# Kernel optimization log

Hardware: AMD Instinct MI355X
Metric: run time of the kernel (lower is better)

The kernel has to match this reference:

```python
import jax, jax.numpy as jnp
import numpy as np

B, S, K, N = 2, 4096, 4096, 4096
BLOCKSIZE = 128  # GPTQ group size


def _unpack_rows(q):
    # int32 [K//8, N] -> int32 [K, N], 8 nibbles packed along dim 0 (little-endian)
    shifts = (jnp.arange(8, dtype=jnp.int32) * 4)
    nib = (q[:, None, :] >> shifts[None, :, None]) & 0xF  # [K//8, 8, N]
    return nib.reshape(q.shape[0] * 8, q.shape[1])


def _unpack_cols(q):
    # int32 [G, N//8] -> int32 [G, N], 8 nibbles packed along dim 1
    shifts = (jnp.arange(8, dtype=jnp.int32) * 4)
    nib = (q[:, :, None] >> shifts[None, None, :]) & 0xF  # [G, N//8, 8]
    return nib.reshape(q.shape[0], q.shape[1] * 8)


def _dequant(qweight, scales, qzeros, blocksize):
    # GPTQ int4 dequant: w[k, n] = (q[k, n] - z[g, n]) * s[g, n], g = k // blocksize
    w_int = _unpack_rows(qweight).astype(jnp.float32)          # [K, N]
    zeros = _unpack_cols(qzeros).astype(jnp.float32)           # [G, N]
    z = jnp.repeat(zeros, blocksize, axis=0)                   # [K, N]
    s = jnp.repeat(scales, blocksize, axis=0)                  # [K, N]
    return (w_int - z) * s


def setup_inputs() -> dict:
    key = jax.random.key(0)
    ks = jax.random.split(key, 6)
    inp = jax.random.normal(ks[0], (B, S, K), dtype=jnp.float32)
    residual = jax.random.normal(ks[1], (B, S, N), dtype=jnp.float32)
    qweight = jax.random.randint(ks[2], (K // 8, N), 0, 2147483647, dtype=jnp.int32)
    qzeros = jax.random.randint(ks[3], (K // BLOCKSIZE, N // 8), 0, 2147483647, dtype=jnp.int32)
    scales = jax.random.uniform(ks[4], (K // BLOCKSIZE, N), dtype=jnp.float32, minval=1e-3, maxval=1e-2)
    bias = jax.random.normal(ks[5], (N,), dtype=jnp.float32)
    return {"input": inp, "residual": residual, "qweight": qweight,
            "scales": scales, "qzeros": qzeros, "bias": bias}


def reference(input, residual, qweight, scales, qzeros, bias):
    # Fused: dequant(int4 GPTQ) -> GEMM -> +bias -> +residual (mm_bias_add_int4)
    w = _dequant(qweight, scales, qzeros, BLOCKSIZE)           # [K, N]
    out = jnp.einsum('bsk,kn->bsn', input, w) + bias + residual
    return out
```

## Files before the change

### kernel.cpp

```cpp
#include <hip/hip_runtime.h>
#include <hip/hip_bf16.h>
#include <stdint.h>

using bf16 = __hip_bfloat16;
typedef __attribute__((ext_vector_type(8))) short short8;
typedef __attribute__((ext_vector_type(4))) float floatx4;

#define DEVINL __device__ __forceinline__

constexpr int K_DIM = 4096;
constexpr int N_DIM = 4096;
constexpr int M_DIM = 8192;

constexpr int BM = 128, BN = 128, BK = 64;
constexpr int NBLK_N = N_DIM / BN;
constexpr int NBLK_M = M_DIM / BM;

DEVINL void gload_lds16(const void* g, void* l) {
  __builtin_amdgcn_global_load_lds((const __attribute__((address_space(1))) void*)g,
                                   (__attribute__((address_space(3))) void*)l,
                                   16, 0, 0);
}

__global__ __launch_bounds__(256) void k_a_convert(const float* __restrict__ a,
                                                   bf16* __restrict__ o) {
  int t = blockIdx.x * 256 + threadIdx.x;
  const float4* a4 = (const float4*)a;
  float4 v0 = a4[2 * t], v1 = a4[2 * t + 1];
  bf16 h[8];
  h[0] = __float2bfloat16(v0.x); h[1] = __float2bfloat16(v0.y);
  h[2] = __float2bfloat16(v0.z); h[3] = __float2bfloat16(v0.w);
  h[4] = __float2bfloat16(v1.x); h[5] = __float2bfloat16(v1.y);
  h[6] = __float2bfloat16(v1.z); h[7] = __float2bfloat16(v1.w);
  ((uint4*)o)[t] = *(const uint4*)h;
}

__global__ __launch_bounds__(256) void k_dequant(const int* __restrict__ qw,
                                                 const float* __restrict__ scales,
                                                 const int* __restrict__ qz,
                                                 bf16* __restrict__ wt) {
  __shared__ __align__(16) uint4 lds[32 * 8];
  const int b = blockIdx.x;
  const int kp0 = (b & 63) * 8;
  const int n0  = (b >> 6) * 32;
  const int t = threadIdx.x;
  const int n_l = t & 31, kp_l = t >> 5;
  const int n = n0 + n_l, kp = kp0 + kp_l;

  int q = qw[kp * N_DIM + n];
  int g = kp0 >> 4;
  float s = scales[g * N_DIM + n];
  int zword = qz[g * (N_DIM / 8) + (n >> 3)];
  float z = (float)((zword >> ((n & 7) * 4)) & 0xF);
  float nzs = -z * s;
  bf16 h[8];
#pragma unroll
  for (int i = 0; i < 8; ++i) {
    float w = fmaf((float)((q >> (4 * i)) & 0xF), s, nzs);
    h[i] = __float2bfloat16(w);
  }
  lds[n_l * 8 + (kp_l ^ (n_l & 7))] = *(const uint4*)h;
  __syncthreads();
  const int n_o = t >> 3, kp_o = t & 7;
  uint4 v = lds[n_o * 8 + (kp_o ^ (n_o & 7))];
  ((uint4*)wt)[(size_t)(n0 + n_o) * (K_DIM / 8) + kp0 + kp_o] = v;
}

template <bool A_IS_BF16>
__global__ __launch_bounds__(256, 2) void k_gemm(const void* __restrict__ a_ptr,
                                                 const bf16* __restrict__ wt,
                                                 const float* __restrict__ bias,
                                                 const float* __restrict__ residual,
                                                 float* __restrict__ out) {
  __shared__ __align__(16) bf16 As[BM * BK];
  __shared__ __align__(16) bf16 Bs[BN * BK];

  const int tid  = threadIdx.x;
  const int lane = tid & 63;
  const int wave = tid >> 6;
  const int wr = wave >> 1, wc = wave & 1;
  const int quad = lane >> 4, lq = lane & 15;

  const int xcd = blockIdx.x & 7;
  const int idx = blockIdx.x >> 3;
  const int bn = xcd * 4 + (idx & 3);
  const int bm = idx >> 2;
  const int m0 = bm * BM, n0 = bn * BN;

  floatx4 acc[4][4] = {};

  const int st_r8 = lane >> 3;
  const int st_ce = ((lane & 7) ^ (st_r8 & 7)) * 8;

  const int rd_x = lq & 7;

  const bf16*  a_bf = (const bf16*)a_ptr;
  const float* a_f  = (const float*)a_ptr;

  for (int k0 = 0; k0 < K_DIM; k0 += BK) {
    __syncthreads();
#pragma unroll
    for (int j = 0; j < 4; ++j) {
      int g = wave + j * 4;
      const bf16* gp = wt + (size_t)(n0 + g * 8 + st_r8) * K_DIM + k0 + st_ce;
      gload_lds16(gp, &Bs[g * 512]);
    }
    if (A_IS_BF16) {
#pragma unroll
      for (int j = 0; j < 4; ++j) {
        int g = wave + j * 4;
        const bf16* gp = a_bf + (size_t)(m0 + g * 8 + st_r8) * K_DIM + k0 + st_ce;
        gload_lds16(gp, &As[g * 512]);
      }
    } else {
      int row = tid >> 1, half = tid & 1;
      int rx = row & 7;
      const float* srcf = a_f + (size_t)(m0 + row) * K_DIM + k0 + half * 32;
#pragma unroll
      for (int cc = 0; cc < 4; ++cc) {
        int logc = half * 4 + cc;
        float4 v0 = ((const float4*)srcf)[cc * 2];
        float4 v1 = ((const float4*)srcf)[cc * 2 + 1];
        bf16 h[8];
        h[0] = __float2bfloat16(v0.x); h[1] = __float2bfloat16(v0.y);
        h[2] = __float2bfloat16(v0.z); h[3] = __float2bfloat16(v0.w);
        h[4] = __float2bfloat16(v1.x); h[5] = __float2bfloat16(v1.y);
        h[6] = __float2bfloat16(v1.z); h[7] = __float2bfloat16(v1.w);
        *(uint4*)&As[row * BK + ((logc ^ rx) * 8)] = *(const uint4*)h;
      }
    }
    __syncthreads();

#pragma unroll
    for (int s = 0; s < 2; ++s) {
      short8 afr[4], bfr[4];
#pragma unroll
      for (int mi = 0; mi < 4; ++mi)
        afr[mi] = *(const short8*)&As[(wr * 64 + mi * 16 + lq) * BK +
                                      (((s * 4 + quad) ^ rd_x) * 8)];
#pragma unroll
      for (int ni = 0; ni < 4; ++ni)
        bfr[ni] = *(const short8*)&Bs[(wc * 64 + ni * 16 + lq) * BK +
                                      (((s * 4 + quad) ^ rd_x) * 8)];
#pragma unroll
      for (int mi = 0; mi < 4; ++mi)
#pragma unroll
        for (int ni = 0; ni < 4; ++ni)
          acc[mi][ni] = __builtin_amdgcn_mfma_f32_16x16x32_bf16(afr[mi], bfr[ni],
                                                                acc[mi][ni], 0, 0, 0);
    }
  }

#pragma unroll
  for (int ni = 0; ni < 4; ++ni) {
    int col = n0 + wc * 64 + ni * 16 + lq;
    float bv = bias[col];
#pragma unroll
    for (int mi = 0; mi < 4; ++mi) {
      int rbase = m0 + wr * 64 + mi * 16 + quad * 4;
#pragma unroll
      for (int r = 0; r < 4; ++r) {
        size_t idxo = (size_t)(rbase + r) * N_DIM + col;
        out[idxo] = acc[mi][ni][r] + bv + residual[idxo];
      }
    }
  }
}

extern "C" void kernel_launch(void* const* d_in, const int* in_sizes, int n_in,
                              void* d_out, int out_size, void* d_ws, size_t ws_size,
                              hipStream_t stream) {
  const float* input    = (const float*)d_in[0];
  const float* residual = (const float*)d_in[1];
  const int*   qweight  = (const int*)d_in[2];
  const float* scales   = (const float*)d_in[3];
  const int*   qzeros   = (const int*)d_in[4];
  const float* bias     = (const float*)d_in[5];
  float* out = (float*)d_out;

  const size_t wt_bytes = (size_t)N_DIM * K_DIM * sizeof(bf16);
  const size_t a_bytes  = (size_t)M_DIM * K_DIM * sizeof(bf16);

  bf16* wt = (bf16*)d_ws;
  k_dequant<<<64 * 128, 256, 0, stream>>>(qweight, scales, qzeros, wt);

  if (ws_size >= wt_bytes + a_bytes) {
    bf16* a_bf = (bf16*)((char*)d_ws + wt_bytes);
    k_a_convert<<<(M_DIM * K_DIM / 8) / 256, 256, 0, stream>>>(input, a_bf);
    k_gemm<true><<<NBLK_M * NBLK_N, 256, 0, stream>>>(a_bf, wt, bias, residual, out);
  } else {
    k_gemm<false><<<NBLK_M * NBLK_N, 256, 0, stream>>>(input, wt, bias, residual, out);
  }
}
```

Baseline: 598.2 us.

## Add 256x256 double-buffered 8-wave GEMM and merge prep kernels

Replaces the 128x128 single-buffered GEMM with a 256x256-tile, 512-thread kernel. It double-buffers LDS, overlaps global-to-LDS loads with MFMA phases under explicit vmcnt waits, barriers and setprio, and uses an XCD-aware block mapping. It also merges the weight dequant and activation conversion into one launch. The aim is to raise data reuse per tile, hide memory latency behind compute and cut one kernel launch. In exchange the kernel uses much more LDS and registers, and its hand-scheduled waits are fragile.

```diff
diff --git a/kernel.cpp b/kernel.cpp
--- a/kernel.cpp
+++ b/kernel.cpp
@@ -11,10 +11,6 @@
 constexpr int K_DIM = 4096;
 constexpr int N_DIM = 4096;
 constexpr int M_DIM = 8192;
-
-constexpr int BM = 128, BN = 128, BK = 64;
-constexpr int NBLK_N = N_DIM / BN;
-constexpr int NBLK_M = M_DIM / BM;
 
 DEVINL void gload_lds16(const void* g, void* l) {
   __builtin_amdgcn_global_load_lds((const __attribute__((address_space(1))) void*)g,
@@ -22,49 +18,54 @@
                                    16, 0, 0);
 }
 
-__global__ __launch_bounds__(256) void k_a_convert(const float* __restrict__ a,
-                                                   bf16* __restrict__ o) {
-  int t = blockIdx.x * 256 + threadIdx.x;
-  const float4* a4 = (const float4*)a;
-  float4 v0 = a4[2 * t], v1 = a4[2 * t + 1];
-  bf16 h[8];
-  h[0] = __float2bfloat16(v0.x); h[1] = __float2bfloat16(v0.y);
-  h[2] = __float2bfloat16(v0.z); h[3] = __float2bfloat16(v0.w);
-  h[4] = __float2bfloat16(v1.x); h[5] = __float2bfloat16(v1.y);
-  h[6] = __float2bfloat16(v1.z); h[7] = __float2bfloat16(v1.w);
-  ((uint4*)o)[t] = *(const uint4*)h;
-}
-
-__global__ __launch_bounds__(256) void k_dequant(const int* __restrict__ qw,
-                                                 const float* __restrict__ scales,
-                                                 const int* __restrict__ qz,
-                                                 bf16* __restrict__ wt) {
-  __shared__ __align__(16) uint4 lds[32 * 8];
-  const int b = blockIdx.x;
-  const int kp0 = (b & 63) * 8;
-  const int n0  = (b >> 6) * 32;
-  const int t = threadIdx.x;
-  const int n_l = t & 31, kp_l = t >> 5;
-  const int n = n0 + n_l, kp = kp0 + kp_l;
-
-  int q = qw[kp * N_DIM + n];
-  int g = kp0 >> 4;
-  float s = scales[g * N_DIM + n];
-  int zword = qz[g * (N_DIM / 8) + (n >> 3)];
-  float z = (float)((zword >> ((n & 7) * 4)) & 0xF);
-  float nzs = -z * s;
-  bf16 h[8];
-#pragma unroll
-  for (int i = 0; i < 8; ++i) {
-    float w = fmaf((float)((q >> (4 * i)) & 0xF), s, nzs);
-    h[i] = __float2bfloat16(w);
-  }
-  lds[n_l * 8 + (kp_l ^ (n_l & 7))] = *(const uint4*)h;
-  __syncthreads();
-  const int n_o = t >> 3, kp_o = t & 7;
-  uint4 v = lds[n_o * 8 + (kp_o ^ (n_o & 7))];
-  ((uint4*)wt)[(size_t)(n0 + n_o) * (K_DIM / 8) + kp0 + kp_o] = v;
-}
+__global__ __launch_bounds__(256) void k_prep(const int* __restrict__ qw,
+                                              const float* __restrict__ scales,
+                                              const int* __restrict__ qz,
+                                              bf16* __restrict__ wt,
+                                              const float* __restrict__ a,
+                                              bf16* __restrict__ ao) {
+  if (blockIdx.x < 64 * 128) {
+    __shared__ __align__(16) uint4 lds[32 * 8];
+    const int b = blockIdx.x;
+    const int kp0 = (b & 63) * 8;
+    const int n0  = (b >> 6) * 32;
+    const int t = threadIdx.x;
+    const int n_l = t & 31, kp_l = t >> 5;
+    const int n = n0 + n_l, kp = kp0 + kp_l;
+
+    int q = qw[kp * N_DIM + n];
+    int g = kp0 >> 4;
+    float s = scales[g * N_DIM + n];
+    int zword = qz[g * (N_DIM / 8) + (n >> 3)];
+    float z = (float)((zword >> ((n & 7) * 4)) & 0xF);
+    float nzs = -z * s;
+    bf16 h[8];
+#pragma unroll
+    for (int i = 0; i < 8; ++i) {
+      float w = fmaf((float)((q >> (4 * i)) & 0xF), s, nzs);
+      h[i] = __float2bfloat16(w);
+    }
+    lds[n_l * 8 + (kp_l ^ (n_l & 7))] = *(const uint4*)h;
+    __syncthreads();
+    const int n_o = t >> 3, kp_o = t & 7;
+    uint4 v = lds[n_o * 8 + (kp_o ^ (n_o & 7))];
+    ((uint4*)wt)[(size_t)(n0 + n_o) * (K_DIM / 8) + kp0 + kp_o] = v;
+  } else {
+    int t = (blockIdx.x - 64 * 128) * 256 + threadIdx.x;
+    const float4* a4 = (const float4*)a;
+    float4 v0 = a4[2 * t], v1 = a4[2 * t + 1];
+    bf16 h[8];
+    h[0] = __float2bfloat16(v0.x); h[1] = __float2bfloat16(v0.y);
+    h[2] = __float2bfloat16(v0.z); h[3] = __float2bfloat16(v0.w);
+    h[4] = __float2bfloat16(v1.x); h[5] = __float2bfloat16(v1.y);
+    h[6] = __float2bfloat16(v1.z); h[7] = __float2bfloat16(v1.w);
+    ((uint4*)ao)[t] = *(const uint4*)h;
+  }
+}
+
+constexpr int BM = 128, BN = 128, BK = 64;
+constexpr int NBLK_N = N_DIM / BN;
+constexpr int NBLK_M = M_DIM / BM;
 
 template <bool A_IS_BF16>
 __global__ __launch_bounds__(256, 2) void k_gemm(const void* __restrict__ a_ptr,
@@ -91,7 +92,6 @@
 
   const int st_r8 = lane >> 3;
   const int st_ce = ((lane & 7) ^ (st_r8 & 7)) * 8;
-
   const int rd_x = lq & 7;
 
   const bf16*  a_bf = (const bf16*)a_ptr;
@@ -167,6 +167,132 @@
   }
 }
 
+constexpr int TBK = 64;
+constexpr int TNT = K_DIM / TBK;
+
+#define VM4 asm volatile("s_waitcnt vmcnt(4)" ::: "memory")
+#define VM0 asm volatile("s_waitcnt vmcnt(0)" ::: "memory")
+#define VMN
+
+#define STAGE_A(buf, half, kt) {                                                   \
+    const bf16* g0_ = A + (size_t)(m0 + (half) * 128 + wave * 16 + st_r) * K_DIM   \
+                        + (kt) * TBK + st_c;                                       \
+    gload_lds16(g0_,             &As[buf][(half) * 128 + wave * 16    ][0]);       \
+    gload_lds16(g0_ + 8 * K_DIM, &As[buf][(half) * 128 + wave * 16 + 8][0]);       \
+  }
+
+#define STAGE_B(buf, half, kt) {                                                   \
+    const bf16* g1_ = Bw + (size_t)(n0 + (half) * 128 + wave * 16 + st_r) * K_DIM  \
+                        + (kt) * TBK + st_c;                                       \
+    gload_lds16(g1_,             &Bs[buf][(half) * 128 + wave * 16    ][0]);       \
+    gload_lds16(g1_ + 8 * K_DIM, &Bs[buf][(half) * 128 + wave * 16 + 8][0]);       \
+  }
+
+#define PHASE(cur, qm, qn, STG)                                                    \
+  {                                                                                \
+    short8 afr[4][2], bfr[2][2];                                                   \
+    _Pragma("unroll") for (int mi = 0; mi < 4; ++mi) {                             \
+      _Pragma("unroll") for (int s = 0; s < 2; ++s)                                \
+        afr[mi][s] = *(const short8*)&As[cur][(qm) * 128 + wm * 64 + mi * 16 + l15]\
+                                        [rdc[s]];                                  \
+    }                                                                              \
+    _Pragma("unroll") for (int ni = 0; ni < 2; ++ni) {                             \
+      _Pragma("unroll") for (int s = 0; s < 2; ++s)                                \
+        bfr[ni][s] = *(const short8*)&Bs[cur][(qn) * 128 + wn * 32 + ni * 16 + l15]\
+                                        [rdc[s]];                                  \
+    }                                                                              \
+    STG;                                                                           \
+    __builtin_amdgcn_sched_barrier(0);                                             \
+    __builtin_amdgcn_s_barrier();                                                  \
+    __builtin_amdgcn_s_setprio(1);                                                 \
+    _Pragma("unroll") for (int mi = 0; mi < 4; ++mi) {                             \
+      _Pragma("unroll") for (int ni = 0; ni < 2; ++ni) {                           \
+        acc[qm][qn][mi][ni] = __builtin_amdgcn_mfma_f32_16x16x32_bf16(             \
+            afr[mi][0], bfr[ni][0], acc[qm][qn][mi][ni], 0, 0, 0);                 \
+        acc[qm][qn][mi][ni] = __builtin_amdgcn_mfma_f32_16x16x32_bf16(             \
+            afr[mi][1], bfr[ni][1], acc[qm][qn][mi][ni], 0, 0, 0);                 \
+      }                                                                            \
+    }                                                                              \
+    __builtin_amdgcn_s_setprio(0);                                                 \
+    __builtin_amdgcn_sched_barrier(0);                                             \
+  }
+
+#define TILE(cur, SHI, SLO, thi, tlo, VMW)                                         \
+  PHASE(cur, 0, 0, if (SHI) STAGE_A((cur) ^ 1, 1, thi))                            \
+  __builtin_amdgcn_s_barrier();                                                    \
+  PHASE(cur, 0, 1, if (SHI) STAGE_B((cur) ^ 1, 1, thi))                            \
+  __builtin_amdgcn_s_barrier();                                                    \
+  PHASE(cur, 1, 0, if (SLO) STAGE_A((cur), 0, tlo))                                \
+  __builtin_amdgcn_s_barrier();                                                    \
+  PHASE(cur, 1, 1, if (SLO) STAGE_B((cur), 0, tlo))                                \
+  VMW;                                                                             \
+  __builtin_amdgcn_s_barrier();
+
+__global__ __launch_bounds__(512, 2) void k_gemm8(const bf16* __restrict__ A,
+                                                  const bf16* __restrict__ Bw,
+                                                  const float* __restrict__ bias,
+                                                  const float* __restrict__ residual,
+                                                  float* __restrict__ out) {
+  __shared__ __align__(16) bf16 As[2][256][TBK];
+  __shared__ __align__(16) bf16 Bs[2][256][TBK];
+
+  const int tid  = threadIdx.x;
+  const int lane = tid & 63;
+  const int wave = tid >> 6;
+  const int wm = wave >> 2;
+  const int wn = wave & 3;
+  const int quad = lane >> 4, l15 = lane & 15;
+
+  const int wgid = (blockIdx.x & 7) * 64 + (blockIdx.x >> 3);
+  const int bn = (wgid >> 6) * 2 + (wgid & 1);
+  const int bm = (wgid & 63) >> 1;
+  const int m0 = bm * 256, n0 = bn * 256;
+
+  const int st_r = lane >> 3;
+  const int st_c = ((lane & 7) ^ st_r) * 8;
+
+  const int rdc[2] = { ((quad)     ^ (l15 & 7)) * 8,
+                       ((4 + quad) ^ (l15 & 7)) * 8 };
+
+  floatx4 acc[2][2][4][2] = {};
+
+  STAGE_A(0, 0, 0)
+  STAGE_B(0, 0, 0)
+  STAGE_A(0, 1, 0)
+  STAGE_B(0, 1, 0)
+  STAGE_A(1, 0, 1)
+  STAGE_B(1, 0, 1)
+  VM4;
+  __builtin_amdgcn_s_barrier();
+
+#pragma unroll 1
+  for (int t = 0; t < TNT - 2; t += 2) {
+    TILE(0, true, true, t + 1, t + 2, VM4)
+    TILE(1, true, true, t + 2, t + 3, VM4)
+  }
+  TILE(0, true, false, TNT - 1, 0, VM0)
+  TILE(1, false, false, 0, 0, VMN)
+
+#pragma unroll
+  for (int qn = 0; qn < 2; ++qn)
+#pragma unroll
+    for (int ni = 0; ni < 2; ++ni) {
+      int col = n0 + qn * 128 + wn * 32 + ni * 16 + l15;
+      float bv = bias[col];
+#pragma unroll
+      for (int qm = 0; qm < 2; ++qm)
+#pragma unroll
+        for (int mi = 0; mi < 4; ++mi) {
+          int rbase = m0 + qm * 128 + wm * 64 + mi * 16 + quad * 4;
+#pragma unroll
+          for (int r = 0; r < 4; ++r) {
+            size_t o = (size_t)(rbase + r) * N_DIM + col;
+            out[o] = acc[qm][qn][mi][ni][r] + bv + residual[o];
+          }
+        }
+    }
+}
+
 extern "C" void kernel_launch(void* const* d_in, const int* in_sizes, int n_in,
                               void* d_out, int out_size, void* d_ws, size_t ws_size,
                               hipStream_t stream) {
@@ -182,13 +308,15 @@
   const size_t a_bytes  = (size_t)M_DIM * K_DIM * sizeof(bf16);
 
   bf16* wt = (bf16*)d_ws;
-  k_dequant<<<64 * 128, 256, 0, stream>>>(qweight, scales, qzeros, wt);
 
   if (ws_size >= wt_bytes + a_bytes) {
     bf16* a_bf = (bf16*)((char*)d_ws + wt_bytes);
-    k_a_convert<<<(M_DIM * K_DIM / 8) / 256, 256, 0, stream>>>(input, a_bf);
-    k_gemm<true><<<NBLK_M * NBLK_N, 256, 0, stream>>>(a_bf, wt, bias, residual, out);
+    k_prep<<<64 * 128 + (M_DIM * K_DIM / 8) / 256, 256, 0, stream>>>(
+        qweight, scales, qzeros, wt, input, a_bf);
+    k_gemm8<<<(M_DIM / 256) * (N_DIM / 256), 512, 0, stream>>>(
+        a_bf, wt, bias, residual, out);
   } else {
+    k_prep<<<64 * 128, 256, 0, stream>>>(qweight, scales, qzeros, wt, input, nullptr);
     k_gemm<false><<<NBLK_M * NBLK_N, 256, 0, stream>>>(input, wt, bias, residual, out);
   }
 }
```

Result: slower. 645.9 us (+8.0%).

## Add 256x256 eight-wave ping-pong GEMM and merge prep kernels into one launch

Applied to the files above, without the earlier changes.

Replaces the 128x128 single-buffered GEMM with a 256x256 tile, 512-thread kernel. It double-buffers LDS and interleaves global-to-LDS prefetch of the next tiles with MFMA quadrants, using explicit waitcnt, sched barriers and setprio. The dequant and activation-convert kernels are merged into one persistent-style launch to cut launch count and tail effects. Risks include heavy LDS use (128KB per block), register pressure from the larger accumulator set, and fragile hand-placed wait counts.

```diff
diff --git a/kernel.cpp b/kernel.cpp
--- a/kernel.cpp
+++ b/kernel.cpp
@@ -11,10 +11,6 @@
 constexpr int K_DIM = 4096;
 constexpr int N_DIM = 4096;
 constexpr int M_DIM = 8192;
-
-constexpr int BM = 128, BN = 128, BK = 64;
-constexpr int NBLK_N = N_DIM / BN;
-constexpr int NBLK_M = M_DIM / BM;
 
 DEVINL void gload_lds16(const void* g, void* l) {
   __builtin_amdgcn_global_load_lds((const __attribute__((address_space(1))) void*)g,
@@ -22,49 +18,59 @@
                                    16, 0, 0);
 }
 
-__global__ __launch_bounds__(256) void k_a_convert(const float* __restrict__ a,
-                                                   bf16* __restrict__ o) {
-  int t = blockIdx.x * 256 + threadIdx.x;
-  const float4* a4 = (const float4*)a;
-  float4 v0 = a4[2 * t], v1 = a4[2 * t + 1];
-  bf16 h[8];
-  h[0] = __float2bfloat16(v0.x); h[1] = __float2bfloat16(v0.y);
-  h[2] = __float2bfloat16(v0.z); h[3] = __float2bfloat16(v0.w);
-  h[4] = __float2bfloat16(v1.x); h[5] = __float2bfloat16(v1.y);
-  h[6] = __float2bfloat16(v1.z); h[7] = __float2bfloat16(v1.w);
-  ((uint4*)o)[t] = *(const uint4*)h;
-}
-
-__global__ __launch_bounds__(256) void k_dequant(const int* __restrict__ qw,
-                                                 const float* __restrict__ scales,
-                                                 const int* __restrict__ qz,
-                                                 bf16* __restrict__ wt) {
-  __shared__ __align__(16) uint4 lds[32 * 8];
-  const int b = blockIdx.x;
-  const int kp0 = (b & 63) * 8;
-  const int n0  = (b >> 6) * 32;
-  const int t = threadIdx.x;
-  const int n_l = t & 31, kp_l = t >> 5;
-  const int n = n0 + n_l, kp = kp0 + kp_l;
-
-  int q = qw[kp * N_DIM + n];
-  int g = kp0 >> 4;
-  float s = scales[g * N_DIM + n];
-  int zword = qz[g * (N_DIM / 8) + (n >> 3)];
-  float z = (float)((zword >> ((n & 7) * 4)) & 0xF);
-  float nzs = -z * s;
-  bf16 h[8];
-#pragma unroll
-  for (int i = 0; i < 8; ++i) {
-    float w = fmaf((float)((q >> (4 * i)) & 0xF), s, nzs);
-    h[i] = __float2bfloat16(w);
-  }
-  lds[n_l * 8 + (kp_l ^ (n_l & 7))] = *(const uint4*)h;
-  __syncthreads();
-  const int n_o = t >> 3, kp_o = t & 7;
-  uint4 v = lds[n_o * 8 + (kp_o ^ (n_o & 7))];
-  ((uint4*)wt)[(size_t)(n0 + n_o) * (K_DIM / 8) + kp0 + kp_o] = v;
-}
+__global__ __launch_bounds__(256) void k_prep(const int* __restrict__ qw,
+                                              const float* __restrict__ scales,
+                                              const int* __restrict__ qz,
+                                              bf16* __restrict__ wt,
+                                              const float* __restrict__ a,
+                                              bf16* __restrict__ ao) {
+  if (blockIdx.x < 1024) {
+    __shared__ __align__(16) uint4 lds[32 * 8];
+    const int t = threadIdx.x;
+    const int n_l = t & 31, kp_l = t >> 5;
+    const int n_o = t >> 3, kp_o = t & 7;
+#pragma unroll 1
+    for (int j = 0; j < 8; ++j) {
+      const int jb = blockIdx.x + j * 1024;
+      const int kp0 = (jb & 63) * 8;
+      const int n0  = (jb >> 6) * 32;
+      const int n = n0 + n_l, kp = kp0 + kp_l;
+      int q = qw[kp * N_DIM + n];
+      int g = kp0 >> 4;
+      float s = scales[g * N_DIM + n];
+      int zword = qz[g * (N_DIM / 8) + (n >> 3)];
+      float z = (float)((zword >> ((n & 7) * 4)) & 0xF);
+      float nzs = -z * s;
+      bf16 h[8];
+#pragma unroll
+      for (int i = 0; i < 8; ++i)
+        h[i] = __float2bfloat16(fmaf((float)((q >> (4 * i)) & 0xF), s, nzs));
+      lds[n_l * 8 + (kp_l ^ (n_l & 7))] = *(const uint4*)h;
+      __syncthreads();
+      uint4 v = lds[n_o * 8 + (kp_o ^ (n_o & 7))];
+      ((uint4*)wt)[(size_t)(n0 + n_o) * (K_DIM / 8) + kp0 + kp_o] = v;
+      __syncthreads();
+    }
+  } else if (ao) {
+    const int base = (blockIdx.x - 1024) * 256 + threadIdx.x;
+    const float4* a4 = (const float4*)a;
+#pragma unroll 1
+    for (int j = 0; j < 16; ++j) {
+      int t = base + j * 262144;
+      float4 v0 = a4[2 * t], v1 = a4[2 * t + 1];
+      bf16 h[8];
+      h[0] = __float2bfloat16(v0.x); h[1] = __float2bfloat16(v0.y);
+      h[2] = __float2bfloat16(v0.z); h[3] = __float2bfloat16(v0.w);
+      h[4] = __float2bfloat16(v1.x); h[5] = __float2bfloat16(v1.y);
+      h[6] = __float2bfloat16(v1.z); h[7] = __float2bfloat16(v1.w);
+      ((uint4*)ao)[t] = *(const uint4*)h;
+    }
+  }
+}
+
+constexpr int BM = 128, BN = 128, BK = 64;
+constexpr int NBLK_N = N_DIM / BN;
+constexpr int NBLK_M = M_DIM / BM;
 
 template <bool A_IS_BF16>
 __global__ __launch_bounds__(256, 2) void k_gemm(const void* __restrict__ a_ptr,
@@ -91,7 +97,6 @@
 
   const int st_r8 = lane >> 3;
   const int st_ce = ((lane & 7) ^ (st_r8 & 7)) * 8;
-
   const int rd_x = lq & 7;
 
   const bf16*  a_bf = (const bf16*)a_ptr;
@@ -167,6 +172,138 @@
   }
 }
 
+constexpr int TBK = 64;
+constexpr int TNT = K_DIM / TBK;
+
+#define SB0   __builtin_amdgcn_sched_barrier(0)
+#define SBAR  __builtin_amdgcn_s_barrier()
+#define PRIO1 __builtin_amdgcn_s_setprio(1)
+#define PRIO0 __builtin_amdgcn_s_setprio(0)
+#define LGKM0 asm volatile("s_waitcnt lgkmcnt(0)" ::: "memory")
+#define LGKM8 asm volatile("s_waitcnt lgkmcnt(8)" ::: "memory")
+#define VMW4  asm volatile("s_waitcnt vmcnt(4)" ::: "memory")
+#define VMW0  asm volatile("s_waitcnt vmcnt(0)" ::: "memory")
+
+#define ST_A(b, h, kt) {                                                      \
+    const bf16* g_ = A + (size_t)(m0 + (h) * 128 + wave * 16 + st_r) * K_DIM  \
+                       + (kt) * TBK + st_c;                                   \
+    gload_lds16(g_,             &As[b][h][wave * 16    ][0]);                 \
+    gload_lds16(g_ + 8 * K_DIM, &As[b][h][wave * 16 + 8][0]);                 \
+  }
+
+#define ST_B(b, h, kt) {                                                      \
+    const bf16* g_ = Bw + (size_t)(n0 + (h) * 128 + wave * 16 + st_r) * K_DIM \
+                       + (kt) * TBK + st_c;                                   \
+    gload_lds16(g_,             &Bs[b][h][wave * 16    ][0]);                 \
+    gload_lds16(g_ + 8 * K_DIM, &Bs[b][h][wave * 16 + 8][0]);                 \
+  }
+
+#define RD_A(c, qm)                                                           \
+  _Pragma("unroll") for (int mi = 0; mi < 4; ++mi)                            \
+    _Pragma("unroll") for (int s = 0; s < 2; ++s)                             \
+      aS[mi][s] = *(const short8*)&As[c][qm][wm * 64 + mi * 16 + l15][rdc[s]];
+
+#define RD_B(c, qn)                                                           \
+  _Pragma("unroll") for (int ni = 0; ni < 2; ++ni)                            \
+    _Pragma("unroll") for (int s = 0; s < 2; ++s)                             \
+      bS[ni][s] = *(const short8*)                                            \
+          &Bs[c][bh][br0 + (qn) * 32 + ni * 16 + l15][rdc[s]];
+
+#define MFMA16(qm, qn)                                                        \
+  _Pragma("unroll") for (int s = 0; s < 2; ++s)                               \
+    _Pragma("unroll") for (int mi = 0; mi < 4; ++mi)                          \
+      _Pragma("unroll") for (int ni = 0; ni < 2; ++ni)                        \
+        acc[qm][qn][mi][ni] = __builtin_amdgcn_mfma_f32_16x16x32_bf16(        \
+            aS[mi][s], bS[ni][s], acc[qm][qn][mi][ni], 0, 0, 0);
+
+#define TILE(c, t, STB, STA, WMACRO)                                          \
+  {                                                                           \
+    short8 aS[4][2], bS[2][2];                                                \
+                                                             \
+    RD_A(c, 0) RD_B(c, 0)                                                     \
+    if (STB) ST_B((c) ^ 1, 0, (t) + 1)                                        \
+    SB0; LGKM8; SBAR; LGKM0; SB0;                                             \
+    PRIO1; MFMA16(0, 0) PRIO0; SB0; SBAR;                                     \
+                                             \
+    RD_B(c, 1)                                                                \
+    if (STB) ST_B((c) ^ 1, 1, (t) + 1)                                        \
+    SB0; SBAR; LGKM0; SB0;                                                    \
+    PRIO1; MFMA16(0, 1) PRIO0; SB0; SBAR;                                     \
+                                                             \
+    RD_A(c, 1) RD_B(c, 0)                                                     \
+    if (STA) ST_A(c, 0, (t) + 2)                                              \
+    SB0; LGKM8; SBAR; LGKM0; SB0;                                             \
+    PRIO1; MFMA16(1, 0) PRIO0; SB0; SBAR;                                     \
+                                                             \
+    RD_B(c, 1)                                                                \
+    if (STA) ST_A(c, 1, (t) + 2)                                              \
+    SB0; SBAR; LGKM0; SB0;                                                    \
+    PRIO1; MFMA16(1, 1) PRIO0; SB0; WMACRO; SBAR;                             \
+  }
+
+__global__ __launch_bounds__(512, 2) void k_gemm8(const bf16* __restrict__ A,
+                                                  const bf16* __restrict__ Bw,
+                                                  const float* __restrict__ bias,
+                                                  const float* __restrict__ residual,
+                                                  float* __restrict__ out) {
+  __shared__ __align__(16) bf16 As[2][2][128][TBK];
+  __shared__ __align__(16) bf16 Bs[2][2][128][TBK];
+
+  const int tid  = threadIdx.x;
+  const int lane = tid & 63;
+  const int wave = tid >> 6;
+  const int wm = wave >> 2;
+  const int wn = wave & 3;
+  const int quad = lane >> 4, l15 = lane & 15;
+  const int bh  = wn >> 1;
+  const int br0 = (wn & 1) * 64;
+
+  const int wgid = (blockIdx.x & 7) * 64 + (blockIdx.x >> 3);
+  const int bn = (wgid >> 6) * 2 + (wgid & 1);
+  const int bm = (wgid & 63) >> 1;
+  const int m0 = bm * 256, n0 = bn * 256;
+
+  const int st_r = lane >> 3;
+  const int st_c = ((lane & 7) ^ st_r) * 8;
+
+  const int rdc[2] = { ((quad)     ^ (l15 & 7)) * 8,
+                       ((4 + quad) ^ (l15 & 7)) * 8 };
+
+  floatx4 acc[2][2][4][2] = {};
+
+  ST_B(0, 0, 0) ST_B(0, 1, 0)
+  ST_A(0, 0, 0) ST_A(0, 1, 0)
+  ST_A(1, 0, 1) ST_A(1, 1, 1)
+  VMW4; SBAR;
+
+#pragma unroll 1
+  for (int t = 0; t < TNT - 2; t += 2) {
+    TILE(0, t,     1, 1, VMW4)
+    TILE(1, t + 1, 1, 1, VMW4)
+  }
+  TILE(0, TNT - 2, 1, 0, VMW0)
+  TILE(1, TNT - 1, 0, 0, )
+
+#pragma unroll
+  for (int qn = 0; qn < 2; ++qn)
+#pragma unroll
+    for (int ni = 0; ni < 2; ++ni) {
+      int col = n0 + bh * 128 + br0 + qn * 32 + ni * 16 + l15;
+      float bv = bias[col];
+#pragma unroll
+      for (int qm = 0; qm < 2; ++qm)
+#pragma unroll
+        for (int mi = 0; mi < 4; ++mi) {
+          int rbase = m0 + qm * 128 + wm * 64 + mi * 16 + quad * 4;
+#pragma unroll
+          for (int r = 0; r < 4; ++r) {
+            size_t o = (size_t)(rbase + r) * N_DIM + col;
+            out[o] = acc[qm][qn][mi][ni][r] + bv + residual[o];
+          }
+        }
+    }
+}
+
 extern "C" void kernel_launch(void* const* d_in, const int* in_sizes, int n_in,
                               void* d_out, int out_size, void* d_ws, size_t ws_size,
                               hipStream_t stream) {
@@ -182,13 +319,14 @@
   const size_t a_bytes  = (size_t)M_DIM * K_DIM * sizeof(bf16);
 
   bf16* wt = (bf16*)d_ws;
-  k_dequant<<<64 * 128, 256, 0, stream>>>(qweight, scales, qzeros, wt);
 
   if (ws_size >= wt_bytes + a_bytes) {
     bf16* a_bf = (bf16*)((char*)d_ws + wt_bytes);
-    k_a_convert<<<(M_DIM * K_DIM / 8) / 256, 256, 0, stream>>>(input, a_bf);
-    k_gemm<true><<<NBLK_M * NBLK_N, 256, 0, stream>>>(a_bf, wt, bias, residual, out);
+    k_prep<<<2048, 256, 0, stream>>>(qweight, scales, qzeros, wt, input, a_bf);
+    k_gemm8<<<(M_DIM / 256) * (N_DIM / 256), 512, 0, stream>>>(
+        a_bf, wt, bias, residual, out);
   } else {
+    k_prep<<<1024, 256, 0, stream>>>(qweight, scales, qzeros, wt, input, nullptr);
     k_gemm<false><<<NBLK_M * NBLK_N, 256, 0, stream>>>(input, wt, bias, residual, out);
   }
 }
```

Measured after the change: 588.2 us. No clear change (-1.7%).
